# Kernel tuning notes

Measured on AMD Instinct MI355X. Metric: run time of the kernel, lower is better.

The kernel has to match this reference:

```python
import jax, jax.numpy as jnp
import numpy as np

SAMPLERATE = 22050
N_OCTAVES = 16
N_SAMPLES = 32768
MIN_FREQ = 20.0 / (SAMPLERATE // 2)
MAX_FREQ = 3000.0 / (SAMPLERATE // 2)
FREQ_RANGE = MAX_FREQ - MIN_FREQ
BASE_RESONANCE = 0.01


def max_norm(x, axis=-1, eps=1e-8):
    return x / (jnp.max(jnp.abs(x), axis=axis, keepdims=True) + eps)


def exponential_decay(decay_values, n_octaves):
    # decay_values: (B, E, 1). Note the original applies sigmoid here on top of
    # the sigmoid already applied in forward (sigmoid_decay=True) -> double sigmoid.
    dv = jax.nn.sigmoid(decay_values)  # (B, E, 1)
    resonance_factor = (1.0 - BASE_RESONANCE) * 0.99
    decay = BASE_RESONANCE + dv * resonance_factor  # (B, E, 1)
    logd = jnp.log(decay + 1e-12)
    b, e, _ = decay_values.shape
    # cumsum of a per-(b,e) constant over octaves, then exp (matches torch code;
    # F.interpolate to size==n_octaves is the identity here)
    logd = jnp.broadcast_to(logd, (b, e, n_octaves))
    return jnp.exp(jnp.cumsum(logd, axis=-1))  # (B, E, O)


def setup_inputs() -> dict:
    key = jax.random.key(0)
    k1, k2, k3 = jax.random.split(key, 3)
    B, E = 8, 64
    return {
        "f0": jax.random.uniform(k1, (B, E, 1), dtype=jnp.float32),
        "decay_coefficients": jax.random.normal(k2, (B, E, 1), dtype=jnp.float32),
        "unused": jnp.zeros((B, E, 1), dtype=jnp.float32),
        "freq_spacing": jax.random.uniform(k3, (B, E, 1), dtype=jnp.float32),
    }


def reference(f0, decay_coefficients, unused, freq_spacing):
    b, e, _ = f0.shape
    O, S = N_OCTAVES, N_SAMPLES

    f0 = jnp.abs(f0)  # (B, E, 1)
    # sigmoid_decay=True path: sigmoid applied before exponential_decay
    exp_decays = exponential_decay(jax.nn.sigmoid(decay_coefficients), O)  # (B, E, O)

    f0 = (MIN_FREQ + f0 * FREQ_RANGE) * jnp.pi  # (B, E, 1)

    # freq_spacing repeated over octaves then cumsum -> per-octave factors
    factors = jnp.cumsum(jnp.broadcast_to(freq_spacing, (b, e, O)), axis=-1)
    f0s = f0 * factors  # (B, E, O)

    # nyquist cutoff
    f0s = f0s * (f0s < 1.0)

    # phase: cumsum over samples of constant per-octave frequency (faithful to torch)
    phase = jnp.cumsum(jnp.broadcast_to(f0s[..., None], (b, e, O, S)), axis=-1)
    osc = jnp.sin(phase)  # (B, E, O, S)

    osc = osc * exp_decays[..., None]
    osc = jnp.sum(osc, axis=2)  # (B, E, S)
    return max_norm(osc, axis=-1)
```

## Files before the change

kernel.cpp:

```cpp
#include <hip/hip_runtime.h>
#include <math.h>

#define N_OCT  16
#define NS     32768
#define TPB    256
#define NSPLIT 4
#define CHUNK  (NS / NSPLIT)
#define SPT    (CHUNK / TPB)
#define N_BE   512
#define NBLK   (N_BE * NSPLIT)

typedef float v2f __attribute__((ext_vector_type(2)));
typedef _Float16 h4 __attribute__((ext_vector_type(4)));

static __device__ __forceinline__ v2f fma2(v2f a, v2f b, v2f c) {
    return __builtin_elementwise_fma(a, b, c);
}

#define WS_STAGE(ws) ((_Float16*)(ws))
#define WS_MAX(ws)   ((float*)((char*)(ws) + (size_t)N_BE * NS * 2))


static __device__ __forceinline__ void make_consts(
    int be, int t,
    const float* __restrict__ f0_in, const float* __restrict__ dc_in,
    const float* __restrict__ fs_in,
    unsigned int* __restrict__ sRQ,
    float* __restrict__ sCH, float* __restrict__ sCL,
    float* __restrict__ sAMP, int* __restrict__ sLive)
{
    if (t < N_OCT) {
        const int o = t;
        const float f0a = fabsf(f0_in[be]);
        const float dc  = dc_in[be];
        const float fs  = fs_in[be];

        const float MINF = (float)(20.0 / 11025.0);
        const float FRNG = (float)(3000.0 / 11025.0 - 20.0 / 11025.0);

        const float s1    = 1.0f / (1.0f + __expf(-dc));
        const float dv    = 1.0f / (1.0f + __expf(-s1));
        const float decay = 0.01f + dv * 0.9801f;
        const float logd  = __logf(decay + 1e-12f);
        const float f0r   = (MINF + f0a * FRNG) * 3.14159274101257324f;

        float cl = 0.f, cf = 0.f;
        for (int i = 0; i <= o; ++i) { cl += logd; cf += fs; }
        float ed  = __expf(cl);
        float f0s = f0r * cf;
        float a   = ed;
        const bool live = (f0s < 1.0f);
        if (!live) { a = 0.0f; f0s = 0.0f; }

        unsigned long long lm = __ballot(live);
        if (o == 0) *sLive = __popcll(lm);

        const double inv2pi = 0.15915494309189535;
        const double r = (double)f0s * inv2pi;
        const unsigned int rq = (unsigned int)llrint(r * 4294967296.0);

        double drev = r * (double)TPB;
        drev -= floor(drev);
        double c2d = 2.0 * cos(drev * 6.283185307179586);
        float  ch  = (float)c2d;

        sRQ[o]  = rq;
        sCH[o]  = ch;
        sCL[o]  = (float)(c2d - (double)ch);
        sAMP[o] = a;
    }
}

static __device__ __forceinline__ float q32_phase(int n, unsigned int rq)
{
    const unsigned int frac = (unsigned int)n * rq;
    return (float)frac * 2.3283064365386963e-10f;
}

template<int NP>
static __device__ __forceinline__ float body_stage(
    int base, int t,
    const unsigned int* __restrict__ sRQ,
    const float* __restrict__ sCH, const float* __restrict__ sCL,
    const float* __restrict__ sAMP,
    _Float16* __restrict__ stage)
{
    v2f xp[NP], xc[NP], c2h[NP], c2l[NP];

    const int n1 = base + t + 1;
    const int n0 = base + t + 1 - TPB;
    #pragma unroll
    for (int o = 0; o < 2 * NP; ++o) {
        const unsigned int rq = sRQ[o];
        const float a = sAMP[o];
        float xcur  = a * __builtin_amdgcn_sinf(q32_phase(n1, rq));
        float xprev = a * __builtin_amdgcn_sinf(q32_phase(n0, rq));
        const int j = o >> 1;
        if ((o & 1) == 0) {
            xc[j].x = xcur;    xp[j].x = xprev;
            c2h[j].x = sCH[o]; c2l[j].x = sCL[o];
        } else {
            xc[j].y = xcur;    xp[j].y = xprev;
            c2h[j].y = sCH[o]; c2l[j].y = sCL[o];
        }
    }

    float lmax = 0.0f;
    #pragma unroll 4
    for (int k = 0; k < SPT; ++k) {
        v2f acc2 = (v2f)(0.0f);
        #pragma unroll
        for (int j = 0; j < NP; ++j) {
            acc2 += xc[j];
            v2f xn = fma2(c2h[j], xc[j], fma2(c2l[j], xc[j], -xp[j]));
            xp[j] = xc[j];
            xc[j] = xn;
        }
        const float acc = acc2.x + acc2.y;
        stage[k * TPB + t] = (_Float16)acc;
        lmax = fmaxf(lmax, fabsf(acc));
    }
    return lmax;
}

__global__ __launch_bounds__(TPB)
void f0res_stage_k(const float* __restrict__ f0_in,
                   const float* __restrict__ dc_in,
                   const float* __restrict__ fs_in,
                   void* __restrict__ ws)
{
    __shared__ unsigned int sRQ[N_OCT];
    __shared__ float sCH[N_OCT], sCL[N_OCT], sAMP[N_OCT];
    __shared__ float wmax[TPB / 64];
    __shared__ int   sLive;

    const int bid = blockIdx.x;
    const int be  = bid >> 2;
    const int q   = bid & 3;
    const int t   = threadIdx.x;
    const int base = q * CHUNK;

    make_consts(be, t, f0_in, dc_in, fs_in, sRQ, sCH, sCL, sAMP, &sLive);
    __syncthreads();

    const int L  = sLive;
    _Float16* __restrict__ stage = WS_STAGE(ws) + (size_t)be * NS + base;

    float lmax = 0.0f;
    if (L == 0) {
        #pragma unroll
        for (int k = 0; k < SPT; ++k) stage[k * TPB + t] = (_Float16)0.0f;
    } else if (L <= 4) {
        lmax = body_stage<2>(base, t, sRQ, sCH, sCL, sAMP, stage);
    } else if (L <= 8) {
        lmax = body_stage<4>(base, t, sRQ, sCH, sCL, sAMP, stage);
    } else {
        lmax = body_stage<8>(base, t, sRQ, sCH, sCL, sAMP, stage);
    }

    #pragma unroll
    for (int off = 32; off > 0; off >>= 1)
        lmax = fmaxf(lmax, __shfl_down(lmax, off, 64));
    if ((t & 63) == 0) wmax[t >> 6] = lmax;
    __syncthreads();
    if (t == 0) {
        float bmax = wmax[0];
        #pragma unroll
        for (int w = 1; w < TPB / 64; ++w) bmax = fmaxf(bmax, wmax[w]);
        WS_MAX(ws)[bid] = bmax;
    }
}

__global__ __launch_bounds__(TPB)
void f0res_norm_k(const void* __restrict__ ws,
                  float* __restrict__ out)
{
    const int bid = blockIdx.x;
    const int be  = bid >> 2;
    const int q   = bid & 3;
    const int t   = threadIdx.x;

    const float* mx = WS_MAX(ws) + (be << 2);
    const float bmax = fmaxf(fmaxf(mx[0], mx[1]), fmaxf(mx[2], mx[3]));
    const float norm = 1.0f / (bmax + 1e-8f);

    const h4* __restrict__ src =
        (const h4*)(WS_STAGE(ws) + (size_t)be * NS + q * CHUNK);
    float4* __restrict__ dst = (float4*)(out + (size_t)be * NS + q * CHUNK);

    #pragma unroll
    for (int i = 0; i < CHUNK / 4 / TPB; ++i) {
        const int idx = i * TPB + t;
        h4 v = src[idx];
        float4 o;
        o.x = (float)v.x * norm; o.y = (float)v.y * norm;
        o.z = (float)v.z * norm; o.w = (float)v.w * norm;
        dst[idx] = o;
    }
}

extern "C" void kernel_launch(void* const* d_in, const int* in_sizes, int n_in,
                              void* d_out, int out_size, void* d_ws, size_t ws_size,
                              hipStream_t stream) {
    const float* f0 = (const float*)d_in[0];
    const float* dc = (const float*)d_in[1];
    const float* fs = (const float*)d_in[3];
    float* out = (float*)d_out;

    hipLaunchKernelGGL(f0res_stage_k, dim3(NBLK), dim3(TPB), 0, stream,
                       f0, dc, fs, d_ws);
    hipLaunchKernelGGL(f0res_norm_k, dim3(NBLK), dim3(TPB), 0, stream,
                       d_ws, out);
}
```

Measured before the change: 112.9 us.

## Fuse stage and normalize kernels with per-row LDS staging

Combines the two kernels into one. Each 512-thread block now handles a whole (b,e) row, keeps the fp16 samples in 64KB of dynamic shared memory, and takes the row max inside the block before normalizing and writing fp32 output. This drops the global workspace round trip and the second launch. In exchange there are only 512 blocks, large LDS use per block, and each thread runs a recurrence twice as long. The recurrence loop is also unrolled in pairs to avoid register copies.

```diff
diff --git a/kernel.cpp b/kernel.cpp
--- a/kernel.cpp
+++ b/kernel.cpp
@@ -1,14 +1,11 @@
 #include <hip/hip_runtime.h>
 #include <math.h>
 
-#define N_OCT  16
-#define NS     32768
-#define TPB    256
-#define NSPLIT 4
-#define CHUNK  (NS / NSPLIT)
-#define SPT    (CHUNK / TPB)
-#define N_BE   512
-#define NBLK   (N_BE * NSPLIT)
+#define N_OCT 16
+#define NS    32768
+#define TPB   512
+#define SPT   (NS / TPB)
+#define N_BE  512
 
 typedef float v2f __attribute__((ext_vector_type(2)));
 typedef _Float16 h4 __attribute__((ext_vector_type(4)));
@@ -16,9 +13,6 @@
 static __device__ __forceinline__ v2f fma2(v2f a, v2f b, v2f c) {
     return __builtin_elementwise_fma(a, b, c);
 }
-
-#define WS_STAGE(ws) ((_Float16*)(ws))
-#define WS_MAX(ws)   ((float*)((char*)(ws) + (size_t)N_BE * NS * 2))
 
 
 static __device__ __forceinline__ void make_consts(
@@ -79,16 +73,16 @@
 
 template<int NP>
 static __device__ __forceinline__ float body_stage(
-    int base, int t,
+    int t,
     const unsigned int* __restrict__ sRQ,
     const float* __restrict__ sCH, const float* __restrict__ sCL,
     const float* __restrict__ sAMP,
-    _Float16* __restrict__ stage)
+    _Float16* __restrict__ smem)
 {
     v2f xp[NP], xc[NP], c2h[NP], c2l[NP];
 
-    const int n1 = base + t + 1;
-    const int n0 = base + t + 1 - TPB;
+    const int n1 = t + 1;
+    const int n0 = t + 1 - TPB;
     #pragma unroll
     for (int o = 0; o < 2 * NP; ++o) {
         const unsigned int rq = sRQ[o];
@@ -106,96 +100,81 @@
     }
 
     float lmax = 0.0f;
-    #pragma unroll 4
-    for (int k = 0; k < SPT; ++k) {
-        v2f acc2 = (v2f)(0.0f);
+    #pragma unroll 2
+    for (int k = 0; k < SPT; k += 2) {
+        v2f accA = (v2f)(0.0f);
         #pragma unroll
         for (int j = 0; j < NP; ++j) {
-            acc2 += xc[j];
-            v2f xn = fma2(c2h[j], xc[j], fma2(c2l[j], xc[j], -xp[j]));
-            xp[j] = xc[j];
-            xc[j] = xn;
+            accA += xc[j];
+            xp[j] = fma2(c2h[j], xc[j], fma2(c2l[j], xc[j], -xp[j]));
         }
-        const float acc = acc2.x + acc2.y;
-        stage[k * TPB + t] = (_Float16)acc;
-        lmax = fmaxf(lmax, fabsf(acc));
+        v2f accB = (v2f)(0.0f);
+        #pragma unroll
+        for (int j = 0; j < NP; ++j) {
+            accB += xp[j];
+            xc[j] = fma2(c2h[j], xp[j], fma2(c2l[j], xp[j], -xc[j]));
+        }
+        const float a = accA.x + accA.y;
+        const float b = accB.x + accB.y;
+        smem[k * TPB + t]       = (_Float16)a;
+        smem[(k + 1) * TPB + t] = (_Float16)b;
+        lmax = fmaxf(lmax, fmaxf(fabsf(a), fabsf(b)));
     }
     return lmax;
 }
 
-__global__ __launch_bounds__(TPB)
-void f0res_stage_k(const float* __restrict__ f0_in,
-                   const float* __restrict__ dc_in,
-                   const float* __restrict__ fs_in,
-                   void* __restrict__ ws)
+__global__ __launch_bounds__(TPB, 1)
+void f0res_kernel(const float* __restrict__ f0_in,
+                  const float* __restrict__ dc_in,
+                  const float* __restrict__ fs_in,
+                  float* __restrict__ out)
 {
+    extern __shared__ _Float16 smem[];
     __shared__ unsigned int sRQ[N_OCT];
     __shared__ float sCH[N_OCT], sCL[N_OCT], sAMP[N_OCT];
     __shared__ float wmax[TPB / 64];
     __shared__ int   sLive;
 
-    const int bid = blockIdx.x;
-    const int be  = bid >> 2;
-    const int q   = bid & 3;
-    const int t   = threadIdx.x;
-    const int base = q * CHUNK;
+    const int be = blockIdx.x;
+    const int t  = threadIdx.x;
 
     make_consts(be, t, f0_in, dc_in, fs_in, sRQ, sCH, sCL, sAMP, &sLive);
     __syncthreads();
 
-    const int L  = sLive;
-    _Float16* __restrict__ stage = WS_STAGE(ws) + (size_t)be * NS + base;
+    const int L = sLive;
+    float* __restrict__ orow = out + (size_t)be * NS;
 
-    float lmax = 0.0f;
     if (L == 0) {
         #pragma unroll
-        for (int k = 0; k < SPT; ++k) stage[k * TPB + t] = (_Float16)0.0f;
-    } else if (L <= 4) {
-        lmax = body_stage<2>(base, t, sRQ, sCH, sCL, sAMP, stage);
-    } else if (L <= 8) {
-        lmax = body_stage<4>(base, t, sRQ, sCH, sCL, sAMP, stage);
-    } else {
-        lmax = body_stage<8>(base, t, sRQ, sCH, sCL, sAMP, stage);
+        for (int k = 0; k < SPT; ++k) orow[k * TPB + t] = 0.0f;
+        return;
     }
+
+    float lmax;
+    if (L <= 4)      lmax = body_stage<2>(t, sRQ, sCH, sCL, sAMP, smem);
+    else if (L <= 8) lmax = body_stage<4>(t, sRQ, sCH, sCL, sAMP, smem);
+    else             lmax = body_stage<8>(t, sRQ, sCH, sCL, sAMP, smem);
 
     #pragma unroll
     for (int off = 32; off > 0; off >>= 1)
         lmax = fmaxf(lmax, __shfl_down(lmax, off, 64));
     if ((t & 63) == 0) wmax[t >> 6] = lmax;
     __syncthreads();
-    if (t == 0) {
-        float bmax = wmax[0];
-        #pragma unroll
-        for (int w = 1; w < TPB / 64; ++w) bmax = fmaxf(bmax, wmax[w]);
-        WS_MAX(ws)[bid] = bmax;
-    }
-}
+    float bmax = wmax[0];
+    #pragma unroll
+    for (int w = 1; w < TPB / 64; ++w) bmax = fmaxf(bmax, wmax[w]);
 
-__global__ __launch_bounds__(TPB)
-void f0res_norm_k(const void* __restrict__ ws,
-                  float* __restrict__ out)
-{
-    const int bid = blockIdx.x;
-    const int be  = bid >> 2;
-    const int q   = bid & 3;
-    const int t   = threadIdx.x;
-
-    const float* mx = WS_MAX(ws) + (be << 2);
-    const float bmax = fmaxf(fmaxf(mx[0], mx[1]), fmaxf(mx[2], mx[3]));
     const float norm = 1.0f / (bmax + 1e-8f);
 
-    const h4* __restrict__ src =
-        (const h4*)(WS_STAGE(ws) + (size_t)be * NS + q * CHUNK);
-    float4* __restrict__ dst = (float4*)(out + (size_t)be * NS + q * CHUNK);
-
+    float4* __restrict__ out4 = (float4*)orow;
     #pragma unroll
-    for (int i = 0; i < CHUNK / 4 / TPB; ++i) {
+    for (int i = 0; i < NS / 4 / TPB; ++i) {
         const int idx = i * TPB + t;
-        h4 v = src[idx];
+        h4 v = *(const h4*)(smem + 4 * (size_t)idx);
         float4 o;
         o.x = (float)v.x * norm; o.y = (float)v.y * norm;
         o.z = (float)v.z * norm; o.w = (float)v.w * norm;
-        dst[idx] = o;
+        out4[idx] = o;
     }
 }
 
@@ -206,9 +185,8 @@
     const float* dc = (const float*)d_in[1];
     const float* fs = (const float*)d_in[3];
     float* out = (float*)d_out;
+    (void)d_ws; (void)ws_size;
 
-    hipLaunchKernelGGL(f0res_stage_k, dim3(NBLK), dim3(TPB), 0, stream,
-                       f0, dc, fs, d_ws);
-    hipLaunchKernelGGL(f0res_norm_k, dim3(NBLK), dim3(TPB), 0, stream,
-                       d_ws, out);
+    hipLaunchKernelGGL(f0res_kernel, dim3(N_BE), dim3(TPB),
+                       NS * sizeof(_Float16), stream, f0, dc, fs, out);
 }
```

Result: faster. 99.70 us (-11.7%).

## Fuse normalize pass into main kernel via last-block atomic counter

Applied to the files above, without the earlier changes.

Replaces the separate normalization kernel with a last-block-done pattern. Each block publishes its max, increments a per-row atomic counter, and the final block of each row rescales the whole row from fp16 staging to the fp32 output. A tiny init kernel zeroes the counters. The recurrence loop is also unrolled by two with ping-pong register swapping, which removes the xp=xc copies. The main risk is that only one block in four does the normalization, so that tail work is serialized per row.

```diff
diff --git a/kernel.cpp b/kernel.cpp
--- a/kernel.cpp
+++ b/kernel.cpp
@@ -19,6 +19,7 @@
 
 #define WS_STAGE(ws) ((_Float16*)(ws))
 #define WS_MAX(ws)   ((float*)((char*)(ws) + (size_t)N_BE * NS * 2))
+#define WS_DONE(ws)  ((int*)((char*)(ws) + (size_t)N_BE * NS * 2 + 8192))
 
 
 static __device__ __forceinline__ void make_consts(
@@ -106,33 +107,46 @@
     }
 
     float lmax = 0.0f;
-    #pragma unroll 4
-    for (int k = 0; k < SPT; ++k) {
-        v2f acc2 = (v2f)(0.0f);
+    #pragma unroll 2
+    for (int k = 0; k < SPT; k += 2) {
+        v2f accA = (v2f)(0.0f);
         #pragma unroll
         for (int j = 0; j < NP; ++j) {
-            acc2 += xc[j];
-            v2f xn = fma2(c2h[j], xc[j], fma2(c2l[j], xc[j], -xp[j]));
-            xp[j] = xc[j];
-            xc[j] = xn;
+            accA += xc[j];
+            xp[j] = fma2(c2h[j], xc[j], fma2(c2l[j], xc[j], -xp[j]));
         }
-        const float acc = acc2.x + acc2.y;
-        stage[k * TPB + t] = (_Float16)acc;
-        lmax = fmaxf(lmax, fabsf(acc));
+        v2f accB = (v2f)(0.0f);
+        #pragma unroll
+        for (int j = 0; j < NP; ++j) {
+            accB += xp[j];
+            xc[j] = fma2(c2h[j], xp[j], fma2(c2l[j], xp[j], -xc[j]));
+        }
+        const float a = accA.x + accA.y;
+        const float b = accB.x + accB.y;
+        stage[k * TPB + t]       = (_Float16)a;
+        stage[(k + 1) * TPB + t] = (_Float16)b;
+        lmax = fmaxf(lmax, fmaxf(fabsf(a), fabsf(b)));
     }
     return lmax;
 }
 
+__global__ __launch_bounds__(512)
+void f0res_init(void* __restrict__ ws)
+{
+    WS_DONE(ws)[threadIdx.x] = 0;
+}
+
 __global__ __launch_bounds__(TPB)
-void f0res_stage_k(const float* __restrict__ f0_in,
-                   const float* __restrict__ dc_in,
-                   const float* __restrict__ fs_in,
-                   void* __restrict__ ws)
+void f0res_main(const float* __restrict__ f0_in,
+                const float* __restrict__ dc_in,
+                const float* __restrict__ fs_in,
+                void* __restrict__ ws,
+                float* __restrict__ out)
 {
     __shared__ unsigned int sRQ[N_OCT];
     __shared__ float sCH[N_OCT], sCL[N_OCT], sAMP[N_OCT];
     __shared__ float wmax[TPB / 64];
-    __shared__ int   sLive;
+    __shared__ int   sLive, sLast;
 
     const int bid = blockIdx.x;
     const int be  = bid >> 2;
@@ -143,7 +157,7 @@
     make_consts(be, t, f0_in, dc_in, fs_in, sRQ, sCH, sCL, sAMP, &sLive);
     __syncthreads();
 
-    const int L  = sLive;
+    const int L = sLive;
     _Float16* __restrict__ stage = WS_STAGE(ws) + (size_t)be * NS + base;
 
     float lmax = 0.0f;
@@ -163,33 +177,28 @@
         lmax = fmaxf(lmax, __shfl_down(lmax, off, 64));
     if ((t & 63) == 0) wmax[t >> 6] = lmax;
     __syncthreads();
+
     if (t == 0) {
         float bmax = wmax[0];
         #pragma unroll
         for (int w = 1; w < TPB / 64; ++w) bmax = fmaxf(bmax, wmax[w]);
         WS_MAX(ws)[bid] = bmax;
-    }
-}
-
-__global__ __launch_bounds__(TPB)
-void f0res_norm_k(const void* __restrict__ ws,
-                  float* __restrict__ out)
-{
-    const int bid = blockIdx.x;
-    const int be  = bid >> 2;
-    const int q   = bid & 3;
-    const int t   = threadIdx.x;
+        __threadfence();
+        sLast = (atomicAdd(&WS_DONE(ws)[be], 1) == NSPLIT - 1);
+    }
+    __syncthreads();
+    if (!sLast) return;
+
+    __threadfence();
 
     const float* mx = WS_MAX(ws) + (be << 2);
     const float bmax = fmaxf(fmaxf(mx[0], mx[1]), fmaxf(mx[2], mx[3]));
     const float norm = 1.0f / (bmax + 1e-8f);
 
-    const h4* __restrict__ src =
-        (const h4*)(WS_STAGE(ws) + (size_t)be * NS + q * CHUNK);
-    float4* __restrict__ dst = (float4*)(out + (size_t)be * NS + q * CHUNK);
-
-    #pragma unroll
-    for (int i = 0; i < CHUNK / 4 / TPB; ++i) {
+    const h4* __restrict__ src = (const h4*)(WS_STAGE(ws) + (size_t)be * NS);
+    float4* __restrict__ dst = (float4*)(out + (size_t)be * NS);
+    #pragma unroll 4
+    for (int i = 0; i < NS / 4 / TPB; ++i) {
         const int idx = i * TPB + t;
         h4 v = src[idx];
         float4 o;
@@ -207,8 +216,7 @@
     const float* fs = (const float*)d_in[3];
     float* out = (float*)d_out;
 
-    hipLaunchKernelGGL(f0res_stage_k, dim3(NBLK), dim3(TPB), 0, stream,
-                       f0, dc, fs, d_ws);
-    hipLaunchKernelGGL(f0res_norm_k, dim3(NBLK), dim3(TPB), 0, stream,
-                       d_ws, out);
-}
+    hipLaunchKernelGGL(f0res_init, dim3(1), dim3(512), 0, stream, d_ws);
+    hipLaunchKernelGGL(f0res_main, dim3(NBLK), dim3(TPB), 0, stream,
+                       f0, dc, fs, d_ws, out);
+}
```

Result: slower. 360.2 us (+219.0%).
